# Performance work log

Hardware: AMD Instinct MI355X
Metric: run time of the kernel (lower is better)

Reference implementation:

```python
import jax, jax.numpy as jnp
import numpy as np

N = 100000  # num_nodes


def setup_inputs() -> dict:
    key = jax.random.key(0)
    k1, k2, k3, k4 = jax.random.split(key, 4)
    nodes = jax.random.randint(k1, (10000,), 0, N)
    edge_index = jax.random.randint(k2, (2, 1600000), 0, N)
    emb_weight = jax.random.normal(k3, (N, 512), dtype=jnp.float32)
    W = jax.random.normal(k4, (512, 128), dtype=jnp.float32) * 0.05
    return {"nodes": nodes, "edge_index": edge_index, "emb_weight": emb_weight, "W": W}


def reference(nodes, edge_index, emb_weight, W):
    # GCNConv (PyG semantics, bias=False): add self-loops, symmetric deg
    # normalization, linear transform, scatter-add aggregation into targets.
    num_nodes = emb_weight.shape[0]
    loops = jnp.arange(num_nodes, dtype=edge_index.dtype)
    row = jnp.concatenate([edge_index[0], loops])  # sources (x_j)
    col = jnp.concatenate([edge_index[1], loops])  # targets (aggregation)

    ones = jnp.ones(row.shape[0], dtype=emb_weight.dtype)
    deg = jax.ops.segment_sum(ones, col, num_segments=num_nodes)
    dinv = jnp.where(deg > 0, jax.lax.rsqrt(deg), 0.0)
    norm = dinv[row] * dinv[col]  # [E+N]

    h = emb_weight @ W  # [N, C] dense transform (main GEMM)
    msg = h[row] * norm[:, None]  # gather + scale, [E+N, C]
    out = jax.ops.segment_sum(msg, col, num_segments=num_nodes)  # scatter-add
    return out[nodes]
```

## Files before the change

### kernel.cpp

```cpp
#include <hip/hip_runtime.h>
#include <hip/hip_bf16.h>


constexpr int KDIM = 512;
constexpr int CDIM = 128;
constexpr int CAPB = 64;
constexpr int CAPO = 16;

typedef __attribute__((ext_vector_type(8))) short short8;
typedef __attribute__((ext_vector_type(4))) float f32x4;

static __device__ __forceinline__ unsigned short f2bf(float f) {
    __hip_bfloat16 b = __float2bfloat16(f);
    return *reinterpret_cast<unsigned short*>(&b);
}
static __device__ __forceinline__ float bf2f(unsigned short b) {
    return __uint_as_float(((unsigned)b) << 16);
}

__global__ void k_init(int* __restrict__ deg, int* __restrict__ tmap,
                       int* __restrict__ cur, int* __restrict__ ocnt,
                       int* __restrict__ ucount,
                       const float* __restrict__ W, unsigned short* __restrict__ wt,
                       int N, int n) {
    int i = blockIdx.x * blockDim.x + threadIdx.x;
    if (i < N) { deg[i] = 0; tmap[i] = -1; }
    if (i < n) { cur[i] = 0; ocnt[i] = 0; }
    if (i == 0) *ucount = 0;
    if (i < 65536) {
        int j  = i & 7;
        int l  = (i >> 3) & 63;
        int st = i >> 9;
        int t  = st & 7, s = st >> 3;
        int k  = s * 32 + (l >> 4) * 8 + j;
        int c  = t * 16 + (l & 15);
        wt[i] = f2bf(W[(size_t)k * CDIM + c]);
    }
}

__global__ void k_targets(const int* __restrict__ nodes, int n,
                          int* __restrict__ tmap, int* __restrict__ tlist,
                          int* __restrict__ ucount) {
    int i = blockIdx.x * blockDim.x + threadIdx.x;
    if (i >= n) return;
    int v = nodes[i];
    if (atomicCAS(&tmap[v], -1, -2) == -1) {
        int slot = atomicAdd(ucount, 1);
        tlist[slot] = v;
        tmap[v] = slot;
    }
}

__global__ __launch_bounds__(512, 2)
void k_main(const float* __restrict__ emb, const unsigned short* __restrict__ wt,
            unsigned short* __restrict__ h, int N,
            const int* __restrict__ erow, const int* __restrict__ ecol, int E,
            int* __restrict__ deg, const int* __restrict__ tmap,
            int* __restrict__ cur, int* __restrict__ ebuf,
            const int* __restrict__ nodes, int n,
            int* __restrict__ ocnt, int* __restrict__ olist,
            int GB, int DB) {
    int bid = (int)blockIdx.x;
    if (bid >= GB + DB) {
        int i = (bid - GB - DB) * 512 + threadIdx.x;
        if (i >= n) return;
        int slot = tmap[nodes[i]];
        int p = atomicAdd(&ocnt[slot], 1);
        if (p < CAPO) olist[slot * CAPO + p] = i;
        return;
    }
    if (bid >= GB) {
        int t = (bid - GB) * 512 + threadIdx.x;
        int base = t * 4;
        if (base >= E) return;
        if (base + 4 <= E) {
            int4 c = *reinterpret_cast<const int4*>(ecol + base);
            atomicAdd(&deg[c.x], 1);
            atomicAdd(&deg[c.y], 1);
            atomicAdd(&deg[c.z], 1);
            atomicAdd(&deg[c.w], 1);
            int s0 = tmap[c.x], s1 = tmap[c.y], s2 = tmap[c.z], s3 = tmap[c.w];
            if ((s0 >= 0) | (s1 >= 0) | (s2 >= 0) | (s3 >= 0)) {
                int4 r = *reinterpret_cast<const int4*>(erow + base);
                if (s0 >= 0) { int p = atomicAdd(&cur[s0], 1); if (p < CAPB) ebuf[s0 * CAPB + p] = r.x; }
                if (s1 >= 0) { int p = atomicAdd(&cur[s1], 1); if (p < CAPB) ebuf[s1 * CAPB + p] = r.y; }
                if (s2 >= 0) { int p = atomicAdd(&cur[s2], 1); if (p < CAPB) ebuf[s2 * CAPB + p] = r.z; }
                if (s3 >= 0) { int p = atomicAdd(&cur[s3], 1); if (p < CAPB) ebuf[s3 * CAPB + p] = r.w; }
            }
        } else {
            for (int i = base; i < E; ++i) {
                int c = ecol[i];
                atomicAdd(&deg[c], 1);
                int s = tmap[c];
                if (s >= 0) { int p = atomicAdd(&cur[s], 1); if (p < CAPB) ebuf[s * CAPB + p] = erow[i]; }
            }
        }
        return;
    }
    extern __shared__ char smem[];
    float*          sA = (float*)smem;
    unsigned short* sB = (unsigned short*)(smem + 3 * 16384);
    int tid  = threadIdx.x;
    int lane = tid & 63;
    int wid  = tid >> 6;
    int row0 = bid * 128;

    auto stage = [&](int buf, int kc) {
        #pragma unroll
        for (int p = 0; p < 2; ++p) {
            int i = p * 512 + tid;
            int row = i >> 3, chunk = i & 7;
            int swz = chunk ^ (row & 7);
            int rg = row0 + row; if (rg >= N) rg = N - 1;
            const float* g = emb + (size_t)rg * KDIM + kc * 32 + swz * 4;
            float* l = sA + buf * 4096 + i * 4;
            __builtin_amdgcn_global_load_lds(
                (const __attribute__((address_space(1))) void*)g,
                (__attribute__((address_space(3))) void*)l, 16, 0, 0);
        }
        {
            const unsigned short* g = wt + (size_t)kc * 4096 + tid * 8;
            unsigned short* l = sB + buf * 4096 + tid * 8;
            __builtin_amdgcn_global_load_lds(
                (const __attribute__((address_space(1))) void*)g,
                (__attribute__((address_space(3))) void*)l, 16, 0, 0);
        }
    };

    f32x4 acc[8];
    #pragma unroll
    for (int t = 0; t < 8; ++t) acc[t] = (f32x4){0.f, 0.f, 0.f, 0.f};

    int arow = wid * 16 + (lane & 15);
    int kq   = lane >> 4;

    auto compute = [&](int buf) {
        const float*          Ab = sA + buf * 4096;
        const unsigned short* Bb = sB + buf * 4096;
        int c0 = kq * 2;
        int s0 = c0 ^ (arow & 7);
        int s1 = (c0 + 1) ^ (arow & 7);
        float4 v0 = *reinterpret_cast<const float4*>(Ab + arow * 32 + s0 * 4);
        float4 v1 = *reinterpret_cast<const float4*>(Ab + arow * 32 + s1 * 4);
        short8 af;
        af[0] = (short)f2bf(v0.x); af[1] = (short)f2bf(v0.y);
        af[2] = (short)f2bf(v0.z); af[3] = (short)f2bf(v0.w);
        af[4] = (short)f2bf(v1.x); af[5] = (short)f2bf(v1.y);
        af[6] = (short)f2bf(v1.z); af[7] = (short)f2bf(v1.w);
        #pragma unroll
        for (int tt = 0; tt < 8; ++tt) {
            short8 bf = *reinterpret_cast<const short8*>(Bb + ((size_t)(tt * 64 + lane)) * 8);
            acc[tt] = __builtin_amdgcn_mfma_f32_16x16x32_bf16(af, bf, acc[tt], 0, 0, 0);
        }
    };

    stage(0, 0); stage(1, 1); stage(2, 2);

    for (int kc = 0; kc < 14; ++kc) {
        if (kc > 0) stage((kc + 2) % 3, kc + 2);
        asm volatile("s_waitcnt vmcnt(6)" ::: "memory");
        __builtin_amdgcn_s_barrier();
        asm volatile("" ::: "memory");
        compute(kc % 3);
        asm volatile("" ::: "memory");
        __builtin_amdgcn_s_barrier();
    }
    asm volatile("s_waitcnt vmcnt(3)" ::: "memory");
    __builtin_amdgcn_s_barrier();
    asm volatile("" ::: "memory");
    compute(2);
    asm volatile("" ::: "memory");
    __builtin_amdgcn_s_barrier();
    asm volatile("s_waitcnt vmcnt(0)" ::: "memory");
    __builtin_amdgcn_s_barrier();
    asm volatile("" ::: "memory");
    compute(0);

    __syncthreads();
    unsigned short* sC = (unsigned short*)smem;
    int rl0 = wid * 16 + (lane >> 4) * 4;
    int cl0 = lane & 15;
    #pragma unroll
    for (int tt = 0; tt < 8; ++tt)
        #pragma unroll
        for (int j = 0; j < 4; ++j)
            sC[(rl0 + j) * 128 + cl0 + tt * 16] = f2bf(acc[tt][j]);
    __syncthreads();
    #pragma unroll
    for (int c = 0; c < 4; ++c) {
        int i = c * 512 + tid;
        int row = i >> 4, off = i & 15;
        int r = row0 + row;
        if (r < N)
            *reinterpret_cast<short8*>(h + (size_t)r * CDIM + off * 8) =
                *reinterpret_cast<const short8*>(sC + row * 128 + off * 8);
    }
}

__global__ __launch_bounds__(256)
void k_agg(const unsigned short* __restrict__ h, const int* __restrict__ deg,
           const int* __restrict__ tlist, const int* __restrict__ cur,
           const int* __restrict__ ebuf, const int* __restrict__ ucount,
           const int* __restrict__ ocnt, const int* __restrict__ olist,
           float* __restrict__ out) {
    int u = *ucount;
    int slot = blockIdx.x * 4 + (threadIdx.x >> 6);
    if (slot >= u) return;
    int lane = threadIdx.x & 63;
    int e = min(cur[slot], CAPB);
    int myi = 0; float myw = 0.f;
    if (lane < e) {
        myi = ebuf[(size_t)slot * CAPB + lane];
        myw = rsqrtf((float)(deg[myi] + 1));
    }
    int q  = lane >> 4;
    int cl = lane & 15;
    float acc[8];
    #pragma unroll
    for (int x = 0; x < 8; ++x) acc[x] = 0.f;
    int trips = (e + 3) >> 2;
    for (int t = 0; t < trips; ++t) {
        int j = t * 4 + q;
        int   src = __shfl(myi, j, 64);
        float w   = __shfl(myw, j, 64);
        short8 v = *reinterpret_cast<const short8*>(h + (size_t)src * CDIM + cl * 8);
        #pragma unroll
        for (int x = 0; x < 8; ++x)
            acc[x] += w * bf2f((unsigned short)v[x]);
    }
    #pragma unroll
    for (int x = 0; x < 8; ++x) {
        acc[x] += __shfl_xor(acc[x], 16, 64);
        acc[x] += __shfl_xor(acc[x], 32, 64);
    }
    int t = tlist[slot];
    float dt = rsqrtf((float)(deg[t] + 1));
    short8 v = *reinterpret_cast<const short8*>(h + (size_t)t * CDIM + cl * 8);
    float4 r0, r1;
    r0.x = dt * (acc[0] + dt * bf2f((unsigned short)v[0]));
    r0.y = dt * (acc[1] + dt * bf2f((unsigned short)v[1]));
    r0.z = dt * (acc[2] + dt * bf2f((unsigned short)v[2]));
    r0.w = dt * (acc[3] + dt * bf2f((unsigned short)v[3]));
    r1.x = dt * (acc[4] + dt * bf2f((unsigned short)v[4]));
    r1.y = dt * (acc[5] + dt * bf2f((unsigned short)v[5]));
    r1.z = dt * (acc[6] + dt * bf2f((unsigned short)v[6]));
    r1.w = dt * (acc[7] + dt * bf2f((unsigned short)v[7]));
    if (q == 0) {
        int cnt = min(ocnt[slot], CAPO);
        for (int qq = 0; qq < cnt; ++qq) {
            int i = olist[slot * CAPO + qq];
            float* op = out + (size_t)i * CDIM + cl * 8;
            *reinterpret_cast<float4*>(op)     = r0;
            *reinterpret_cast<float4*>(op + 4) = r1;
        }
    }
}

extern "C" void kernel_launch(void* const* d_in, const int* in_sizes, int n_in,
                              void* d_out, int out_size, void* d_ws, size_t ws_size,
                              hipStream_t stream) {
    const int*   nodes = (const int*)d_in[0];
    const int*   eidx  = (const int*)d_in[1];
    const float* emb   = (const float*)d_in[2];
    const float* W     = (const float*)d_in[3];
    float*       out   = (float*)d_out;

    int n = in_sizes[0];
    int E = in_sizes[1] / 2;
    int N = in_sizes[2] / KDIM;
    const int* erow = eidx;
    const int* ecol = eidx + E;

    char* ws = (char*)d_ws;
    size_t o = 0;
    auto carve = [&](size_t bytes) {
        char* p = ws + o;
        o = (o + bytes + 255) & ~(size_t)255;
        return p;
    };
    int* deg    = (int*)carve((size_t)N * 4);
    int* tmap   = (int*)carve((size_t)N * 4);
    int* tlist  = (int*)carve((size_t)n * 4);
    int* cur    = (int*)carve((size_t)n * 4);
    int* ocnt   = (int*)carve((size_t)n * 4);
    int* olist  = (int*)carve((size_t)n * CAPO * 4);
    int* ucount = (int*)carve(4);
    int* ebuf   = (int*)carve((size_t)n * CAPB * 4);
    unsigned short* wt = (unsigned short*)carve((size_t)16 * 8 * 64 * 8 * 2);
    unsigned short* h  = (unsigned short*)carve((size_t)N * CDIM * 2);
    (void)ws_size; (void)n_in; (void)out_size;

    hipFuncSetAttribute(reinterpret_cast<const void*>(k_main),
                        hipFuncAttributeMaxDynamicSharedMemorySize, 73728);

    int GB = (N + 127) / 128;
    int DB = (E + 2047) / 2048;
    int OB = (n + 511) / 512;
    k_init   <<<(N + 255) / 256, 256, 0, stream>>>(deg, tmap, cur, ocnt, ucount, W, wt, N, n);
    k_targets<<<(n + 255) / 256, 256, 0, stream>>>(nodes, n, tmap, tlist, ucount);
    k_main   <<<GB + DB + OB, 512, 73728, stream>>>(emb, wt, h, N,
                                                    erow, ecol, E, deg, tmap, cur, ebuf,
                                                    nodes, n, ocnt, olist, GB, DB);
    k_agg    <<<(n + 3) / 4, 256, 0, stream>>>(h, deg, tlist, cur, ebuf, ucount,
                                               ocnt, olist, out);
}
```

Before: 130.6 us.

## Use per-wave A staging and direct global W reads to drop block barriers

Shrinks GEMM blocks to 256 threads and 64 rows. Each wave now stages its own 16 rows of embedding into static LDS, so the main loop needs only waitcnt and no block-wide barriers. The B operand (bf16 W) is read directly from global/L2 instead of being staged in LDS, which cuts LDS use and should raise occupancy. The trade-off is more global traffic for W, and the epilogue reuses a 24KB buffer that must still hold the 64x128 bf16 tile.

```diff
diff --git a/kernel.cpp b/kernel.cpp
--- a/kernel.cpp
+++ b/kernel.cpp
@@ -51,7 +51,7 @@
     }
 }
 
-__global__ __launch_bounds__(512, 2)
+__global__ __launch_bounds__(256, 4)
 void k_main(const float* __restrict__ emb, const unsigned short* __restrict__ wt,
             unsigned short* __restrict__ h, int N,
             const int* __restrict__ erow, const int* __restrict__ ecol, int E,
@@ -60,9 +60,11 @@
             const int* __restrict__ nodes, int n,
             int* __restrict__ ocnt, int* __restrict__ olist,
             int GB, int DB) {
+    __shared__ float sA[3][64 * 32];
     int bid = (int)blockIdx.x;
+    int tid = threadIdx.x;
     if (bid >= GB + DB) {
-        int i = (bid - GB - DB) * 512 + threadIdx.x;
+        int i = (bid - GB - DB) * 256 + tid;
         if (i >= n) return;
         int slot = tmap[nodes[i]];
         int p = atomicAdd(&ocnt[slot], 1);
@@ -70,7 +72,7 @@
         return;
     }
     if (bid >= GB) {
-        int t = (bid - GB) * 512 + threadIdx.x;
+        int t = (bid - GB) * 256 + tid;
         int base = t * 4;
         if (base >= E) return;
         if (base + 4 <= E) {
@@ -97,87 +99,62 @@
         }
         return;
     }
-    extern __shared__ char smem[];
-    float*          sA = (float*)smem;
-    unsigned short* sB = (unsigned short*)(smem + 3 * 16384);
-    int tid  = threadIdx.x;
     int lane = tid & 63;
     int wid  = tid >> 6;
-    int row0 = bid * 128;
+    int row0 = bid * 64;
 
     auto stage = [&](int buf, int kc) {
         #pragma unroll
         for (int p = 0; p < 2; ++p) {
-            int i = p * 512 + tid;
-            int row = i >> 3, chunk = i & 7;
+            int s = p * 64 + lane;
+            int row = s >> 3, chunk = s & 7;
             int swz = chunk ^ (row & 7);
-            int rg = row0 + row; if (rg >= N) rg = N - 1;
+            int rg = row0 + wid * 16 + row; if (rg >= N) rg = N - 1;
             const float* g = emb + (size_t)rg * KDIM + kc * 32 + swz * 4;
-            float* l = sA + buf * 4096 + i * 4;
+            float* l = &sA[buf][(wid * 16 + row) * 32 + chunk * 4];
             __builtin_amdgcn_global_load_lds(
                 (const __attribute__((address_space(1))) void*)g,
                 (__attribute__((address_space(3))) void*)l, 16, 0, 0);
         }
-        {
-            const unsigned short* g = wt + (size_t)kc * 4096 + tid * 8;
-            unsigned short* l = sB + buf * 4096 + tid * 8;
-            __builtin_amdgcn_global_load_lds(
-                (const __attribute__((address_space(1))) void*)g,
-                (__attribute__((address_space(3))) void*)l, 16, 0, 0);
-        }
     };
 
     f32x4 acc[8];
     #pragma unroll
     for (int t = 0; t < 8; ++t) acc[t] = (f32x4){0.f, 0.f, 0.f, 0.f};
 
-    int arow = wid * 16 + (lane & 15);
-    int kq   = lane >> 4;
-
-    auto compute = [&](int buf) {
-        const float*          Ab = sA + buf * 4096;
-        const unsigned short* Bb = sB + buf * 4096;
+    int arl = lane & 15;
+    int al  = wid * 16 + arl;
+    int kq  = lane >> 4;
+
+    stage(0, 0); stage(1, 1); stage(2, 2);
+
+    for (int kc = 0; kc < 16; ++kc) {
+        if (kc > 0 && kc + 2 < 16) stage((kc + 2) % 3, kc + 2);
+        if (kc < 14)       asm volatile("s_waitcnt vmcnt(4)" ::: "memory");
+        else if (kc == 14) asm volatile("s_waitcnt vmcnt(2)" ::: "memory");
+        else               asm volatile("s_waitcnt vmcnt(0)" ::: "memory");
+        const float* Ab = sA[kc % 3];
         int c0 = kq * 2;
-        int s0 = c0 ^ (arow & 7);
-        int s1 = (c0 + 1) ^ (arow & 7);
-        float4 v0 = *reinterpret_cast<const float4*>(Ab + arow * 32 + s0 * 4);
-        float4 v1 = *reinterpret_cast<const float4*>(Ab + arow * 32 + s1 * 4);
+        int p0 = c0 ^ (arl & 7);
+        int p1 = (c0 + 1) ^ (arl & 7);
+        float4 v0 = *reinterpret_cast<const float4*>(Ab + al * 32 + p0 * 4);
+        float4 v1 = *reinterpret_cast<const float4*>(Ab + al * 32 + p1 * 4);
         short8 af;
         af[0] = (short)f2bf(v0.x); af[1] = (short)f2bf(v0.y);
         af[2] = (short)f2bf(v0.z); af[3] = (short)f2bf(v0.w);
         af[4] = (short)f2bf(v1.x); af[5] = (short)f2bf(v1.y);
         af[6] = (short)f2bf(v1.z); af[7] = (short)f2bf(v1.w);
+        const short8* wp = reinterpret_cast<const short8*>(wt)
+                         + (size_t)(kc * 8) * 64 + lane;
         #pragma unroll
         for (int tt = 0; tt < 8; ++tt) {
-            short8 bf = *reinterpret_cast<const short8*>(Bb + ((size_t)(tt * 64 + lane)) * 8);
+            short8 bf = wp[tt * 64];
             acc[tt] = __builtin_amdgcn_mfma_f32_16x16x32_bf16(af, bf, acc[tt], 0, 0, 0);
         }
-    };
-
-    stage(0, 0); stage(1, 1); stage(2, 2);
-
-    for (int kc = 0; kc < 14; ++kc) {
-        if (kc > 0) stage((kc + 2) % 3, kc + 2);
-        asm volatile("s_waitcnt vmcnt(6)" ::: "memory");
-        __builtin_amdgcn_s_barrier();
-        asm volatile("" ::: "memory");
-        compute(kc % 3);
-        asm volatile("" ::: "memory");
-        __builtin_amdgcn_s_barrier();
-    }
-    asm volatile("s_waitcnt vmcnt(3)" ::: "memory");
-    __builtin_amdgcn_s_barrier();
-    asm volatile("" ::: "memory");
-    compute(2);
-    asm volatile("" ::: "memory");
-    __builtin_amdgcn_s_barrier();
-    asm volatile("s_waitcnt vmcnt(0)" ::: "memory");
-    __builtin_amdgcn_s_barrier();
-    asm volatile("" ::: "memory");
-    compute(0);
+    }
 
     __syncthreads();
-    unsigned short* sC = (unsigned short*)smem;
+    unsigned short* sC = (unsigned short*)sA;
     int rl0 = wid * 16 + (lane >> 4) * 4;
     int cl0 = lane & 15;
     #pragma unroll
@@ -188,7 +165,7 @@
     __syncthreads();
     #pragma unroll
     for (int c = 0; c < 4; ++c) {
-        int i = c * 512 + tid;
+        int i = c * 256 + tid;
         int row = i >> 4, off = i & 15;
         int r = row0 + row;
         if (r < N)
@@ -290,17 +267,14 @@
     unsigned short* h  = (unsigned short*)carve((size_t)N * CDIM * 2);
     (void)ws_size; (void)n_in; (void)out_size;
 
-    hipFuncSetAttribute(reinterpret_cast<const void*>(k_main),
-                        hipFuncAttributeMaxDynamicSharedMemorySize, 73728);
-
-    int GB = (N + 127) / 128;
-    int DB = (E + 2047) / 2048;
-    int OB = (n + 511) / 512;
+    int GB = (N + 63) / 64;
+    int DB = (E + 1023) / 1024;
+    int OB = (n + 255) / 256;
     k_init   <<<(N + 255) / 256, 256, 0, stream>>>(deg, tmap, cur, ocnt, ucount, W, wt, N, n);
     k_targets<<<(n + 255) / 256, 256, 0, stream>>>(nodes, n, tmap, tlist, ucount);
-    k_main   <<<GB + DB + OB, 512, 73728, stream>>>(emb, wt, h, N,
-                                                    erow, ecol, E, deg, tmap, cur, ebuf,
-                                                    nodes, n, ocnt, olist, GB, DB);
+    k_main   <<<GB + DB + OB, 256, 0, stream>>>(emb, wt, h, N,
+                                                erow, ecol, E, deg, tmap, cur, ebuf,
+                                                nodes, n, ocnt, olist, GB, DB);
     k_agg    <<<(n + 3) / 4, 256, 0, stream>>>(h, deg, tlist, cur, ebuf, ucount,
                                                ocnt, olist, out);
 }
```

After: 140.8 us. 7.8% more time.
